# Kernel optimization log

Measured on AMD Instinct MI355X. Metric: run time of the kernel, lower is better.

## Reference

```python
import jax, jax.numpy as jnp
import numpy as np

NUM_HEADS = 16
D_MODEL = 1024


def setup_inputs() -> dict:
    key = jax.random.key(0)
    k1, k2 = jax.random.split(key)
    x = jax.random.normal(k1, (4, 2048, D_MODEL), dtype=jnp.float32)
    # kqv Linear(d_model, 3*d_model, bias=False); stored as [in, out] for x @ W
    W_kqv = jax.random.normal(k2, (D_MODEL, 3 * D_MODEL), dtype=jnp.float32) * (D_MODEL ** -0.5)
    return {"x": x, "W_kqv": W_kqv}


def _alibi_slopes(num_heads):
    # 1 / ((2**8)**((i+1)/num_heads)) for each head
    base = (2.0 ** 8) ** (1.0 / num_heads)
    return jnp.asarray([1.0 / base ** (i + 1) for i in range(num_heads)], dtype=jnp.float32)


def reference(x, W_kqv):
    B, S, D = x.shape
    H = NUM_HEADS
    hd = D // H
    scale = jnp.sqrt(jnp.float32(D))  # note: sqrt(d_model), faithful to source

    kqv = x @ W_kqv  # [B, S, 3D]; chunk order in source: key, query, value
    k, q, v = jnp.split(kqv, 3, axis=-1)
    # [B, H, S, hd]
    q = q.reshape(B, S, H, hd).transpose(0, 2, 1, 3)
    k = k.reshape(B, S, H, hd).transpose(0, 2, 1, 3)
    v = v.reshape(B, S, H, hd).transpose(0, 2, 1, 3)

    # ALiBi bias: m[h] * (j - i), shape [1, H, S, S]
    pos = jnp.arange(S)
    rel = (pos[None, :] - pos[:, None]).astype(jnp.float32)  # [S, S]
    m = _alibi_slopes(H)  # [H]
    bias = m[:, None, None] * rel  # [H, S, S]

    score = jnp.einsum('bhsd,bhnd->bhsn', q, k) / scale + bias[None]
    attn = jax.nn.softmax(score, axis=-1)
    out = jnp.einsum('bhsn,bhnd->bhsd', attn, v)  # [B, H, S, hd]
    out = out.transpose(0, 2, 1, 3).reshape(B, S, D)
    return out
```

## Files before the change

### kernel.cpp

```cpp
#include <hip/hip_runtime.h>
#include <stdint.h>

typedef __bf16 bf16;
typedef __bf16 bf16x8 __attribute__((ext_vector_type(8)));
typedef float f32x4 __attribute__((ext_vector_type(4)));

#define AS1 __attribute__((address_space(1)))
#define AS3 __attribute__((address_space(3)))


__global__ void cvt_x_kernel(const float* __restrict__ x, bf16* __restrict__ xb) {
    int i = blockIdx.x * 256 + threadIdx.x;
    const float4* x4 = (const float4*)x;
    float4 a = x4[i * 2];
    float4 b = x4[i * 2 + 1];
    bf16x8 o;
    o[0] = (bf16)a.x; o[1] = (bf16)a.y; o[2] = (bf16)a.z; o[3] = (bf16)a.w;
    o[4] = (bf16)b.x; o[5] = (bf16)b.y; o[6] = (bf16)b.z; o[7] = (bf16)b.w;
    *(bf16x8*)(xb + (size_t)i * 8) = o;
}

__global__ void cvt_w_kernel(const float* __restrict__ w, bf16* __restrict__ wt) {
    __shared__ float tile[32][33];
    int nt = blockIdx.x, kt = blockIdx.y;
    int tx = threadIdx.x, ty = threadIdx.y;
#pragma unroll
    for (int j = 0; j < 4; ++j)
        tile[ty + j * 8][tx] = w[(size_t)(kt * 32 + ty + j * 8) * 3072 + nt * 32 + tx];
    __syncthreads();
#pragma unroll
    for (int j = 0; j < 4; ++j)
        wt[(size_t)(nt * 32 + ty + j * 8) * 1024 + kt * 32 + tx] = (bf16)tile[tx][ty + j * 8];
}

__global__ __launch_bounds__(256) void gemm_kqv_kernel(
    const bf16* __restrict__ xb, const bf16* __restrict__ wt,
    bf16* __restrict__ kb, bf16* __restrict__ qb, bf16* __restrict__ vt) {
    __shared__ bf16 As[2][128 * 32];
    __shared__ bf16 Bs[2][128 * 32];
    int bid = blockIdx.x;
    int bm = bid / 24, bn = bid % 24;
    int m0 = bm * 128, n0 = bn * 128;
    int t = threadIdx.x;
    int lane = t & 63, wid = t >> 6;
    int g = lane >> 4, l15 = lane & 15;
    int wr = wid >> 1, wc = wid & 1;

    f32x4 acc[4][4] = {};

    auto stageAB = [&](int ks, int buf) {
        int k0 = ks * 32;
#pragma unroll
        for (int c = 0; c < 2; ++c) {
            int slot = c * 256 + t;
            int row = slot >> 2, kk = (slot & 3) * 8;
            __builtin_amdgcn_global_load_lds(
                (const AS1 void*)(xb + (size_t)(m0 + row) * 1024 + k0 + kk),
                (AS3 void*)(&As[buf][slot * 8]), 16, 0, 0);
        }
#pragma unroll
        for (int c = 0; c < 2; ++c) {
            int slot = c * 256 + t;
            int row = slot >> 2, kk = (slot & 3) * 8;
            __builtin_amdgcn_global_load_lds(
                (const AS1 void*)(wt + (size_t)(n0 + row) * 1024 + k0 + kk),
                (AS3 void*)(&Bs[buf][slot * 8]), 16, 0, 0);
        }
    };

    stageAB(0, 0);
    for (int ks = 0; ks < 32; ++ks) {
        __syncthreads();
        if (ks + 1 < 32) stageAB(ks + 1, (ks + 1) & 1);
        const bf16* Ab = As[ks & 1];
        const bf16* Bb = Bs[ks & 1];
        bf16x8 af[4], bfr[4];
#pragma unroll
        for (int mi = 0; mi < 4; ++mi)
            af[mi] = *(const bf16x8*)(Ab + (wr * 64 + mi * 16 + l15) * 32 + g * 8);
#pragma unroll
        for (int ni = 0; ni < 4; ++ni)
            bfr[ni] = *(const bf16x8*)(Bb + (wc * 64 + ni * 16 + l15) * 32 + g * 8);
#pragma unroll
        for (int mi = 0; mi < 4; ++mi)
#pragma unroll
            for (int ni = 0; ni < 4; ++ni)
                acc[mi][ni] = __builtin_amdgcn_mfma_f32_16x16x32_bf16(
                    af[mi], bfr[ni], acc[mi][ni], 0, 0, 0);
    }

    int tsel = n0 >> 10;
#pragma unroll
    for (int mi = 0; mi < 4; ++mi) {
#pragma unroll
        for (int ni = 0; ni < 4; ++ni) {
#pragma unroll
            for (int r = 0; r < 4; ++r) {
                int row = m0 + wr * 64 + mi * 16 + g * 4 + r;
                int col = n0 + wc * 64 + ni * 16 + l15;
                int b = row >> 11, s = row & 2047;
                int cc = col & 1023;
                int h = cc >> 6, d = cc & 63;
                int bh = b * 16 + h;
                float v = acc[mi][ni][r];
                if (tsel == 0)      kb[((size_t)bh * 2048 + s) * 64 + d] = (bf16)v;
                else if (tsel == 1) qb[((size_t)bh * 2048 + s) * 64 + d] = (bf16)(v * 0.0450842503f);
                else                vt[((size_t)bh * 64 + d) * 2048 + s] = (bf16)v;
            }
        }
    }
}

__global__ __launch_bounds__(256) void attn_kernel(
    const bf16* __restrict__ qb, const bf16* __restrict__ kb,
    const bf16* __restrict__ vt, float* __restrict__ out) {
    __shared__ bf16 Kl[64 * 64];
    __shared__ bf16 Vl[2][64 * 64];
    __shared__ bf16 Pl[4][32 * 64];
    int bid = blockIdx.x;
    int bh = bid >> 4, qt = bid & 15;
    int b = bh >> 4, h = bh & 15;
    int t = threadIdx.x, lane = t & 63, wid = t >> 6;
    int g = lane >> 4, l15 = lane & 15;
    int q0 = qt * 128 + wid * 32;
    float mh2 = exp2f(-0.5f * (float)(h + 1)) * 1.44269504f;

    const bf16* Qp = qb + ((size_t)bh * 2048 + q0) * 64;
    const bf16* Kp = kb + (size_t)bh * 2048 * 64;
    const bf16* Vp = vt + (size_t)bh * 64 * 2048;

    bf16x8 qf[2][2];
#pragma unroll
    for (int qi = 0; qi < 2; ++qi)
#pragma unroll
        for (int kk = 0; kk < 2; ++kk)
            qf[qi][kk] = *(const bf16x8*)(Qp + (size_t)(qi * 16 + l15) * 64 + kk * 32 + g * 8);

    f32x4 oacc[2][4] = {};
    float mrun[2][4], lrun[2][4];
#pragma unroll
    for (int qi = 0; qi < 2; ++qi)
#pragma unroll
        for (int r = 0; r < 4; ++r) { mrun[qi][r] = -3.0e38f; lrun[qi][r] = 0.f; }

    float colb[4];
#pragma unroll
    for (int ji = 0; ji < 4; ++ji) colb[ji] = mh2 * (float)(ji * 16 + l15);

    auto stageK = [&](int tile) {
        int j0 = tile * 64;
#pragma unroll
        for (int c = 0; c < 2; ++c) {
            int slot = c * 256 + t;
            int row = slot >> 3;
            int cs = (slot & 7) ^ (row & 7);
            __builtin_amdgcn_global_load_lds(
                (const AS1 void*)(Kp + (size_t)(j0 + row) * 64 + cs * 8),
                (AS3 void*)(&Kl[slot * 8]), 16, 0, 0);
        }
    };
    auto stageV = [&](int tile, int buf) {
        int j0 = tile * 64;
#pragma unroll
        for (int c = 0; c < 2; ++c) {
            int slot = c * 256 + t;
            int row = slot >> 3;
            int cs = (slot & 7) ^ (row & 7);
            __builtin_amdgcn_global_load_lds(
                (const AS1 void*)(Vp + (size_t)row * 2048 + j0 + cs * 8),
                (AS3 void*)(&Vl[buf][slot * 8]), 16, 0, 0);
        }
    };

    stageK(0);
    stageV(0, 0);
    bf16* Pw = Pl[wid];

    for (int tile = 0; tile < 32; ++tile) {
        __syncthreads();
        const bf16* Vb = Vl[tile & 1];

        f32x4 sc[2][4] = {};
#pragma unroll
        for (int ji = 0; ji < 4; ++ji) {
#pragma unroll
            for (int kk = 0; kk < 2; ++kk) {
                int row = ji * 16 + l15;
                int c16 = (kk * 4 + g) ^ (row & 7);
                bf16x8 kf = *(const bf16x8*)(Kl + row * 64 + c16 * 8);
#pragma unroll
                for (int qi = 0; qi < 2; ++qi)
                    sc[qi][ji] = __builtin_amdgcn_mfma_f32_16x16x32_bf16(
                        qf[qi][kk], kf, sc[qi][ji], 0, 0, 0);
            }
        }
        __syncthreads();
        if (tile + 1 < 32) {
            stageK(tile + 1);
            stageV(tile + 1, (tile + 1) & 1);
        }

        float tb = mh2 * (float)(tile * 64);
        float pmx[2][4];
#pragma unroll
        for (int qi = 0; qi < 2; ++qi) {
#pragma unroll
            for (int ji = 0; ji < 4; ++ji) {
                float add = tb + colb[ji];
#pragma unroll
                for (int r = 0; r < 4; ++r) sc[qi][ji][r] += add;
            }
#pragma unroll
            for (int r = 0; r < 4; ++r)
                pmx[qi][r] = fmaxf(fmaxf(sc[qi][0][r], sc[qi][1][r]),
                                   fmaxf(sc[qi][2][r], sc[qi][3][r]));
        }

        int stable = 1;
#pragma unroll
        for (int qi = 0; qi < 2; ++qi)
#pragma unroll
            for (int r = 0; r < 4; ++r)
                stable &= (pmx[qi][r] <= mrun[qi][r] + 8.0f) ? 1 : 0;
        if (!__all(stable)) {
#pragma unroll
            for (int qi = 0; qi < 2; ++qi)
#pragma unroll
                for (int r = 0; r < 4; ++r) {
                    float mx = pmx[qi][r];
#pragma unroll
                    for (int m = 1; m < 16; m <<= 1) mx = fmaxf(mx, __shfl_xor(mx, m));
                    float mnew = fmaxf(mrun[qi][r], mx);
                    float corr = __builtin_amdgcn_exp2f(mrun[qi][r] - mnew);
                    mrun[qi][r] = mnew;
                    lrun[qi][r] *= corr;
#pragma unroll
                    for (int di = 0; di < 4; ++di) oacc[qi][di][r] *= corr;
                }
        }

#pragma unroll
        for (int qi = 0; qi < 2; ++qi)
#pragma unroll
            for (int r = 0; r < 4; ++r) {
                float mnew = mrun[qi][r];
                float sum = 0.f;
#pragma unroll
                for (int ji = 0; ji < 4; ++ji) {
                    float p = __builtin_amdgcn_exp2f(sc[qi][ji][r] - mnew);
                    sc[qi][ji][r] = p;
                    sum += p;
                }
#pragma unroll
                for (int m = 1; m < 16; m <<= 1) sum += __shfl_xor(sum, m);
                lrun[qi][r] += sum;
            }

#pragma unroll
        for (int qi = 0; qi < 2; ++qi)
#pragma unroll
            for (int r = 0; r < 4; ++r) {
                int row = qi * 16 + g * 4 + r;
                int rs = row & 7;
#pragma unroll
                for (int ji = 0; ji < 4; ++ji) {
                    int col = ji * 16 + l15;
                    int addr = row * 64 + (((col >> 3) ^ rs) * 8) + (col & 7);
                    Pw[addr] = (bf16)sc[qi][ji][r];
                }
            }

#pragma unroll
        for (int kk = 0; kk < 2; ++kk) {
            bf16x8 pf[2];
#pragma unroll
            for (int qi = 0; qi < 2; ++qi) {
                int row = qi * 16 + l15;
                int c16 = (kk * 4 + g) ^ (row & 7);
                pf[qi] = *(const bf16x8*)(Pw + row * 64 + c16 * 8);
            }
#pragma unroll
            for (int di = 0; di < 4; ++di) {
                int row = di * 16 + l15;
                int c16 = (kk * 4 + g) ^ (row & 7);
                bf16x8 vf = *(const bf16x8*)(Vb + row * 64 + c16 * 8);
#pragma unroll
                for (int qi = 0; qi < 2; ++qi)
                    oacc[qi][di] = __builtin_amdgcn_mfma_f32_16x16x32_bf16(
                        pf[qi], vf, oacc[qi][di], 0, 0, 0);
            }
        }
    }

#pragma unroll
    for (int qi = 0; qi < 2; ++qi) {
#pragma unroll
        for (int r = 0; r < 4; ++r) {
            float inv = 1.0f / lrun[qi][r];
            int s = q0 + qi * 16 + g * 4 + r;
            float* op = out + ((size_t)b * 2048 + s) * 1024 + h * 64;
#pragma unroll
            for (int di = 0; di < 4; ++di)
                op[di * 16 + l15] = oacc[qi][di][r] * inv;
        }
    }
}

extern "C" void kernel_launch(void* const* d_in, const int* in_sizes, int n_in,
                              void* d_out, int out_size, void* d_ws, size_t ws_size,
                              hipStream_t stream) {
    (void)in_sizes; (void)n_in; (void)out_size; (void)ws_size;
    const float* x = (const float*)d_in[0];
    const float* w = (const float*)d_in[1];
    float* out = (float*)d_out;
    char* ws = (char*)d_ws;
    bf16* xb = (bf16*)(ws);
    bf16* wt = (bf16*)(ws + 16777216);
    bf16* kb = (bf16*)(ws + 23068672);
    bf16* qb = (bf16*)(ws + 39845888);
    bf16* vt = (bf16*)(ws + 56623104);

    cvt_x_kernel<<<4096, 256, 0, stream>>>(x, xb);
    cvt_w_kernel<<<dim3(96, 32), dim3(32, 8), 0, stream>>>(w, wt);
    gemm_kqv_kernel<<<1536, 256, 0, stream>>>(xb, wt, kb, qb, vt);
    attn_kernel<<<1024, 256, 0, stream>>>(qb, kb, vt, out);
}
```

Baseline: 376.3 us.

## Transpose QK^T MFMA so each lane owns one query row for softmax

Swaps the MFMA operands so the score tile is computed transposed: each lane holds one query row across 16 keys instead of 4 rows. Row max and row sum then need only two cross-lane shuffles instead of four per row, and the running max and sum state shrinks from 8 to 2 values per lane. The ALiBi bias is preloaded into the accumulator rather than added afterwards, and P is written to LDS as packed 4-element vectors instead of scalar stores. In exchange, the rescale factor and the final normalizer must be broadcast back to the output layout with __shfl, and the P swizzle addressing changes, which adds some risk of indexing mistakes.

```diff
diff --git a/kernel.cpp b/kernel.cpp
--- a/kernel.cpp
+++ b/kernel.cpp
@@ -2,6 +2,7 @@
 #include <stdint.h>
 
 typedef __bf16 bf16;
+typedef __bf16 bf16x4 __attribute__((ext_vector_type(4)));
 typedef __bf16 bf16x8 __attribute__((ext_vector_type(8)));
 typedef float f32x4 __attribute__((ext_vector_type(4)));
 
@@ -137,15 +138,15 @@
             qf[qi][kk] = *(const bf16x8*)(Qp + (size_t)(qi * 16 + l15) * 64 + kk * 32 + g * 8);
 
     f32x4 oacc[2][4] = {};
-    float mrun[2][4], lrun[2][4];
-#pragma unroll
-    for (int qi = 0; qi < 2; ++qi)
-#pragma unroll
-        for (int r = 0; r < 4; ++r) { mrun[qi][r] = -3.0e38f; lrun[qi][r] = 0.f; }
-
-    float colb[4];
-#pragma unroll
-    for (int ji = 0; ji < 4; ++ji) colb[ji] = mh2 * (float)(ji * 16 + l15);
+    float mrun[2], lrun[2];
+    mrun[0] = mrun[1] = -3.0e38f;
+    lrun[0] = lrun[1] = 0.f;
+
+    float jb[4], rb[4];
+#pragma unroll
+    for (int ji = 0; ji < 4; ++ji) jb[ji] = mh2 * (float)(ji * 16 + g * 4);
+#pragma unroll
+    for (int r = 0; r < 4; ++r) rb[r] = mh2 * (float)r;
 
     auto stageK = [&](int tile) {
         int j0 = tile * 64;
@@ -180,7 +181,18 @@
         __syncthreads();
         const bf16* Vb = Vl[tile & 1];
 
-        f32x4 sc[2][4] = {};
+        float tb = mh2 * (float)(tile * 64);
+        f32x4 sc[2][4];
+#pragma unroll
+        for (int ji = 0; ji < 4; ++ji) {
+            float base = tb + jb[ji];
+#pragma unroll
+            for (int r = 0; r < 4; ++r) {
+                float v = base + rb[r];
+                sc[0][ji][r] = v;
+                sc[1][ji][r] = v;
+            }
+        }
 #pragma unroll
         for (int ji = 0; ji < 4; ++ji) {
 #pragma unroll
@@ -191,7 +203,7 @@
 #pragma unroll
                 for (int qi = 0; qi < 2; ++qi)
                     sc[qi][ji] = __builtin_amdgcn_mfma_f32_16x16x32_bf16(
-                        qf[qi][kk], kf, sc[qi][ji], 0, 0, 0);
+                        kf, qf[qi][kk], sc[qi][ji], 0, 0, 0);
             }
         }
         __syncthreads();
@@ -200,84 +212,79 @@
             stageV(tile + 1, (tile + 1) & 1);
         }
 
-        float tb = mh2 * (float)(tile * 64);
-        float pmx[2][4];
+        float pmx[2];
 #pragma unroll
         for (int qi = 0; qi < 2; ++qi) {
+            float m0a = fmaxf(fmaxf(sc[qi][0][0], sc[qi][0][1]), fmaxf(sc[qi][0][2], sc[qi][0][3]));
+            float m1a = fmaxf(fmaxf(sc[qi][1][0], sc[qi][1][1]), fmaxf(sc[qi][1][2], sc[qi][1][3]));
+            float m2a = fmaxf(fmaxf(sc[qi][2][0], sc[qi][2][1]), fmaxf(sc[qi][2][2], sc[qi][2][3]));
+            float m3a = fmaxf(fmaxf(sc[qi][3][0], sc[qi][3][1]), fmaxf(sc[qi][3][2], sc[qi][3][3]));
+            pmx[qi] = fmaxf(fmaxf(m0a, m1a), fmaxf(m2a, m3a));
+        }
+
+        int stable = (pmx[0] <= mrun[0] + 8.0f && pmx[1] <= mrun[1] + 8.0f) ? 1 : 0;
+        if (!__all(stable)) {
+            float corr[2];
+#pragma unroll
+            for (int qi = 0; qi < 2; ++qi) {
+                float mx = pmx[qi];
+                mx = fmaxf(mx, __shfl_xor(mx, 16));
+                mx = fmaxf(mx, __shfl_xor(mx, 32));
+                float mnew = fmaxf(mrun[qi], mx);
+                corr[qi] = __builtin_amdgcn_exp2f(mrun[qi] - mnew);
+                mrun[qi] = mnew;
+                lrun[qi] *= corr[qi];
+            }
+#pragma unroll
+            for (int qi = 0; qi < 2; ++qi)
+#pragma unroll
+                for (int r = 0; r < 4; ++r) {
+                    float cB = __shfl(corr[qi], g * 4 + r);
+#pragma unroll
+                    for (int di = 0; di < 4; ++di) oacc[qi][di][r] *= cB;
+                }
+        }
+
+#pragma unroll
+        for (int qi = 0; qi < 2; ++qi) {
+            float mq = mrun[qi];
+            float s = 0.f;
+#pragma unroll
+            for (int ji = 0; ji < 4; ++ji)
+#pragma unroll
+                for (int r = 0; r < 4; ++r) {
+                    float p = __builtin_amdgcn_exp2f(sc[qi][ji][r] - mq);
+                    sc[qi][ji][r] = p;
+                    s += p;
+                }
+            s += __shfl_xor(s, 16);
+            s += __shfl_xor(s, 32);
+            lrun[qi] += s;
+        }
+
+#pragma unroll
+        for (int qi = 0; qi < 2; ++qi) {
+            int qloc = qi * 16 + l15;
+            int base = qloc * 64;
+            int swz = (qloc & 7) * 8;
 #pragma unroll
             for (int ji = 0; ji < 4; ++ji) {
-                float add = tb + colb[ji];
-#pragma unroll
-                for (int r = 0; r < 4; ++r) sc[qi][ji][r] += add;
-            }
-#pragma unroll
-            for (int r = 0; r < 4; ++r)
-                pmx[qi][r] = fmaxf(fmaxf(sc[qi][0][r], sc[qi][1][r]),
-                                   fmaxf(sc[qi][2][r], sc[qi][3][r]));
-        }
-
-        int stable = 1;
-#pragma unroll
-        for (int qi = 0; qi < 2; ++qi)
-#pragma unroll
-            for (int r = 0; r < 4; ++r)
-                stable &= (pmx[qi][r] <= mrun[qi][r] + 8.0f) ? 1 : 0;
-        if (!__all(stable)) {
-#pragma unroll
-            for (int qi = 0; qi < 2; ++qi)
-#pragma unroll
-                for (int r = 0; r < 4; ++r) {
-                    float mx = pmx[qi][r];
-#pragma unroll
-                    for (int m = 1; m < 16; m <<= 1) mx = fmaxf(mx, __shfl_xor(mx, m));
-                    float mnew = fmaxf(mrun[qi][r], mx);
-                    float corr = __builtin_amdgcn_exp2f(mrun[qi][r] - mnew);
-                    mrun[qi][r] = mnew;
-                    lrun[qi][r] *= corr;
-#pragma unroll
-                    for (int di = 0; di < 4; ++di) oacc[qi][di][r] *= corr;
-                }
-        }
-
-#pragma unroll
-        for (int qi = 0; qi < 2; ++qi)
-#pragma unroll
-            for (int r = 0; r < 4; ++r) {
-                float mnew = mrun[qi][r];
-                float sum = 0.f;
-#pragma unroll
-                for (int ji = 0; ji < 4; ++ji) {
-                    float p = __builtin_amdgcn_exp2f(sc[qi][ji][r] - mnew);
-                    sc[qi][ji][r] = p;
-                    sum += p;
-                }
-#pragma unroll
-                for (int m = 1; m < 16; m <<= 1) sum += __shfl_xor(sum, m);
-                lrun[qi][r] += sum;
-            }
-
-#pragma unroll
-        for (int qi = 0; qi < 2; ++qi)
-#pragma unroll
-            for (int r = 0; r < 4; ++r) {
-                int row = qi * 16 + g * 4 + r;
-                int rs = row & 7;
-#pragma unroll
-                for (int ji = 0; ji < 4; ++ji) {
-                    int col = ji * 16 + l15;
-                    int addr = row * 64 + (((col >> 3) ^ rs) * 8) + (col & 7);
-                    Pw[addr] = (bf16)sc[qi][ji][r];
-                }
-            }
+                bf16x4 pv;
+                pv[0] = (bf16)sc[qi][ji][0];
+                pv[1] = (bf16)sc[qi][ji][1];
+                pv[2] = (bf16)sc[qi][ji][2];
+                pv[3] = (bf16)sc[qi][ji][3];
+                *(bf16x4*)(Pw + base + ((ji * 16 + g * 4) ^ swz)) = pv;
+            }
+        }
 
 #pragma unroll
         for (int kk = 0; kk < 2; ++kk) {
             bf16x8 pf[2];
 #pragma unroll
             for (int qi = 0; qi < 2; ++qi) {
-                int row = qi * 16 + l15;
-                int c16 = (kk * 4 + g) ^ (row & 7);
-                pf[qi] = *(const bf16x8*)(Pw + row * 64 + c16 * 8);
+                int qloc = qi * 16 + l15;
+                pf[qi] = *(const bf16x8*)(Pw + qloc * 64 + ((kk * 32 + g * 8) ^ ((qloc & 7) * 8)));
             }
 #pragma unroll
             for (int di = 0; di < 4; ++di) {
@@ -296,7 +303,8 @@
     for (int qi = 0; qi < 2; ++qi) {
 #pragma unroll
         for (int r = 0; r < 4; ++r) {
-            float inv = 1.0f / lrun[qi][r];
+            float lq = __shfl(lrun[qi], g * 4 + r);
+            float inv = 1.0f / lq;
             int s = q0 + qi * 16 + g * 4 + r;
             float* op = out + ((size_t)b * 2048 + s) * 1024 + h * 64;
 #pragma unroll
```

Measured after the change: 311.7 us. 1.21x faster.
